# Optimization experiments

Hardware: AMD Instinct MI355X
Metric: run time of the kernel (lower is better)

Reference implementation:

```python
import jax, jax.numpy as jnp
import numpy as np

N = 100000
E = 1600000
IN_DIM, HID, H_IN, OUT_DIM, H_OUT = 128, 32, 2, 1, 1
NEG_SLOPE = 0.2


def gat_conv(x, W, a_src, a_dst, b, src, dst, concat):
    """PyG-style GATConv. x:[N,F_in], W:[F_in,H*C], a_*:[H,C], b:[H*C] or [C]."""
    H, C = a_src.shape
    h = (x @ W).reshape(N, H, C)
    asrc = jnp.einsum('nhc,hc->nh', h, a_src)   # [N,H]
    adst = jnp.einsum('nhc,hc->nh', h, a_dst)   # [N,H]
    e = jax.nn.leaky_relu(asrc[src] + adst[dst], NEG_SLOPE)  # [E',H]
    # segment softmax over incoming edges of each destination node
    m = jax.ops.segment_max(e, dst, num_segments=N)
    p = jnp.exp(e - m[dst])
    s = jax.ops.segment_sum(p, dst, num_segments=N)
    alpha = p / s[dst]                           # [E',H]
    out = jax.ops.segment_sum(alpha[:, :, None] * h[src], dst, num_segments=N)  # [N,H,C]
    out = out.reshape(N, H * C) if concat else out.mean(axis=1)
    return out + b


def setup_inputs() -> dict:
    key = jax.random.key(0)
    ks = jax.random.split(key, 16)
    def glorot(k, shape):
        fan = sum(shape[-2:]) if len(shape) > 1 else shape[-1]
        return jax.random.normal(k, shape, jnp.float32) * (2.0 / fan) ** 0.5
    node_attrs = jax.random.normal(ks[0], (N, IN_DIM), jnp.float32)
    edge_index = jax.random.randint(ks[1], (2, E), 0, N, jnp.int64 if jax.config.jax_enable_x64 else jnp.int32)
    params = {
        'W_in':  glorot(ks[2], (IN_DIM, H_IN * HID)),
        'a_src_in': glorot(ks[3], (H_IN, HID)),
        'a_dst_in': glorot(ks[4], (H_IN, HID)),
        'b_in':  jnp.zeros((H_IN * HID,), jnp.float32),
        'W_mid': glorot(ks[5], (H_IN * HID, H_IN * HID)),
        'a_src_mid': glorot(ks[6], (H_IN, HID)),
        'a_dst_mid': glorot(ks[7], (H_IN, HID)),
        'b_mid': jnp.zeros((H_IN * HID,), jnp.float32),
        'W_out': glorot(ks[8], (H_IN * HID, H_OUT * OUT_DIM)),
        'a_src_out': glorot(ks[9], (H_OUT, OUT_DIM)),
        'a_dst_out': glorot(ks[10], (H_OUT, OUT_DIM)),
        'b_out': jnp.zeros((OUT_DIM,), jnp.float32),
    }
    return {'node_attrs': node_attrs, 'edge_index': edge_index, **params}


def reference(node_attrs, edge_index,
              W_in, a_src_in, a_dst_in, b_in,
              W_mid, a_src_mid, a_dst_mid, b_mid,
              W_out, a_src_out, a_dst_out, b_out):
    # add self loops (PyG GATConv default add_self_loops=True)
    loops = jnp.arange(N, dtype=edge_index.dtype)
    src = jnp.concatenate([edge_index[0], loops])
    dst = jnp.concatenate([edge_index[1], loops])

    x = gat_conv(node_attrs, W_in, a_src_in, a_dst_in, b_in, src, dst, True)
    initial_x = x
    x = jax.nn.elu(x)
    for _ in range(6):  # conv_mid reused 6 times with SHARED weights, as in source
        x = gat_conv(x, W_mid, a_src_mid, a_dst_mid, b_mid, src, dst, True) + initial_x
        x = jax.nn.elu(x)
    x = gat_conv(x, W_out, a_src_out, a_dst_out, b_out, src, dst, False)
    return jax.nn.sigmoid(x)
```

## Files before the change

### kernel.cpp

```cpp
#include <hip/hip_runtime.h>
#include <hip/hip_fp16.h>
#include <cmath>

#define NN 100000
#define EE 1600000
#define TOTE (EE + NN)
#define SHIFT 10
#define NBUK 98
#define CAPB 18432
#define SLACK 5632
#define SPAN (TOTE + NBUK * SLACK)
#define PCAP2 40

typedef _Float16 half8_t __attribute__((ext_vector_type(8)));
typedef _Float16 half4_t __attribute__((ext_vector_type(4)));
typedef float float4_t __attribute__((ext_vector_type(4)));

__device__ __forceinline__ float lrelu(float v) { return v > 0.f ? v : 0.2f * v; }

__global__ __launch_bounds__(256) void binA(const int* __restrict__ src, const int* __restrict__ dst,
                                            int* __restrict__ gcur, int* __restrict__ region) {
    __shared__ int cnt[NBUK], gbase[NBUK], pos[NBUK];
    int t = threadIdx.x;
    if (t < NBUK) cnt[t] = 0;
    __syncthreads();
    const int CH = (TOTE + gridDim.x - 1) / gridDim.x;
    int lo = blockIdx.x * CH;
    int hi = lo + CH; if (hi > TOTE) hi = TOTE;
    for (int e = lo + t; e < hi; e += 256) {
        int d = (e < EE) ? dst[e] : (e - EE);
        atomicAdd(&cnt[d >> SHIFT], 1);
    }
    __syncthreads();
    if (t < NBUK) {
        gbase[t] = atomicAdd(&gcur[t], cnt[t]);
        pos[t] = 0;
    }
    __syncthreads();
    for (int e = lo + t; e < hi; e += 256) {
        int s, d;
        if (e < EE) { s = src[e]; d = dst[e]; }
        else        { s = e - EE; d = s; }
        int b = d >> SHIFT;
        int k = atomicAdd(&pos[b], 1);
        region[(size_t)b * CAPB + gbase[b] + k] = (s << SHIFT) | (d & 1023);
    }
}

__global__ __launch_bounds__(1024) void binB(const int* __restrict__ region, const int* __restrict__ gcur,
                                             int2* __restrict__ rng, int* __restrict__ esrc) {
    __shared__ int ncur[1024];
    __shared__ int wsum[16];
    __shared__ int sg[NBUK];
    __shared__ int sBase;
    int b = blockIdx.x, t = threadIdx.x;
    int n0 = b << SHIFT;
    if (t < NBUK) sg[t] = gcur[t];
    ncur[t] = 0;
    __syncthreads();
    if (t == 0) {
        int run = 0;
        for (int bb = 0; bb < b; ++bb) run += sg[bb] + SLACK;
        sBase = run;
    }
    int cntE = gcur[b];
    const int* reg = region + (size_t)b * CAPB;
    __syncthreads();
    for (int i = t; i < cntE; i += 1024)
        atomicAdd(&ncur[reg[i] & 1023], 1);
    int base = sBase;
    __syncthreads();
    int v = ncur[t];
    int vp = (v + 7) & ~7;
    __syncthreads();
    int incl = vp;
    for (int off = 1; off < 64; off <<= 1) {
        int u = __shfl_up(incl, off);
        if ((t & 63) >= off) incl += u;
    }
    if ((t & 63) == 63) wsum[t >> 6] = incl;
    __syncthreads();
    if (t < 16) {
        int w = wsum[t];
        int winc = w;
        for (int off = 1; off < 16; off <<= 1) {
            int u = __shfl_up(winc, off);
            if (t >= off) winc += u;
        }
        wsum[t] = winc - w;
    }
    __syncthreads();
    int excl = incl - vp + wsum[t >> 6];
    int start = base + excl;
    int n = n0 + t;
    if (n < NN) rng[n] = make_int2(start, v);
    ncur[t] = start;
    __syncthreads();
    for (int i = t; i < cntE; i += 1024) {
        int p = reg[i];
        int local = p & 1023;
        int k = atomicAdd(&ncur[local], 1);
        esrc[k] = p >> SHIFT;
    }
    __syncthreads();
    if (n < NN) {
        for (int k = start + v; k < start + vp; ++k) esrc[k] = 0;
    }
}

__global__ __launch_bounds__(256) void degHist(const int2* __restrict__ rng, int* __restrict__ hist) {
    __shared__ int cnt[64];
    int t = threadIdx.x;
    if (t < 64) cnt[t] = 0;
    __syncthreads();
    int n = blockIdx.x * 256 + t;
    if (n < NN) {
        int d = rng[n].y; if (d > 63) d = 63;
        atomicAdd(&cnt[d], 1);
    }
    __syncthreads();
    if (t < 64 && cnt[t]) atomicAdd(&hist[t], cnt[t]);
}

__global__ void degScan(const int* __restrict__ hist, int* __restrict__ off) {
    int t = threadIdx.x;
    int v = hist[t];
    int incl = v;
    for (int o = 1; o < 64; o <<= 1) {
        int u = __shfl_up(incl, o);
        if (t >= o) incl += u;
    }
    off[t] = incl - v;
}

__global__ __launch_bounds__(256) void degSort(const int2* __restrict__ rng, int* __restrict__ off,
                                               int* __restrict__ perm) {
    __shared__ int cnt[64], base[64], pos[64];
    int t = threadIdx.x;
    if (t < 64) cnt[t] = 0;
    __syncthreads();
    int n = blockIdx.x * 256 + t;
    int d = 63;
    if (n < NN) {
        d = rng[n].y; if (d > 63) d = 63;
        atomicAdd(&cnt[d], 1);
    }
    __syncthreads();
    if (t < 64) { base[t] = atomicAdd(&off[t], cnt[t]); pos[t] = 0; }
    __syncthreads();
    if (n < NN) {
        int k = atomicAdd(&pos[d], 1);
        perm[base[d] + k] = n;
    }
}

__global__ __launch_bounds__(256) void mkInvRng(const int* __restrict__ perm, const int2* __restrict__ rng,
                                                int* __restrict__ inv, int2* __restrict__ rng2) {
    int i = blockIdx.x * 256 + threadIdx.x;
    if (i < NN) {
        int p = perm[i];
        inv[p] = i;
        rng2[i] = rng[p];
    }
}

__global__ __launch_bounds__(256) void xlat(const int* __restrict__ esrc, const int* __restrict__ inv,
                                            int* __restrict__ esrc2) {
    int k = blockIdx.x * 256 + threadIdx.x;
    if (k < SPAN) {
        unsigned v = (unsigned)esrc[k];
        if (v >= NN) v = 0;
        esrc2[k] = inv[v];
    }
}

__global__ void prepW(const float* __restrict__ Wg, _Float16* __restrict__ Wp) {
    int t = threadIdx.x;
    for (int i = t; i < 64 * 72; i += 256) {
        int row = i / 72, col = i - row * 72;
        _Float16 v = (_Float16)0.f;
        if (col < 64) {
            int k = (col & 3) * 16 + (col >> 2);
            v = (_Float16)Wg[k * 64 + row];
        }
        Wp[i] = v;
    }
}

template <int K, bool F32IN>
__global__ __launch_bounds__(256) void gemm_attn(const void* __restrict__ Xv, const float* __restrict__ W,
                                                 const float* __restrict__ a_src, const float* __restrict__ a_dst,
                                                 _Float16* __restrict__ H, float* __restrict__ asrc,
                                                 float* __restrict__ adst) {
    __shared__ _Float16 wt[64][K + 8];
    int t = threadIdx.x;
    for (int it = 0; it < K / 16; ++it) {
        int idx4 = it * 256 + t;
        int k = idx4 >> 4;
        int n4 = (idx4 * 4) & 63;
        int ks = F32IN ? k : ((k & 15) * 4 + (k >> 4));
        float4 v = *(const float4*)(W + (size_t)idx4 * 4);
        wt[n4 + 0][ks] = (_Float16)v.x;
        wt[n4 + 1][ks] = (_Float16)v.y;
        wt[n4 + 2][ks] = (_Float16)v.z;
        wt[n4 + 3][ks] = (_Float16)v.w;
    }
    __syncthreads();

    int row0 = blockIdx.x * 64;
    int wr = (t >> 6) * 16;
    int lane = t & 63;
    int m = lane & 15;
    int q = lane >> 4;

    int rowA = row0 + wr + m;
    if (rowA >= NN) rowA = NN - 1;

    float4_t acc[4] = { {0,0,0,0}, {0,0,0,0}, {0,0,0,0}, {0,0,0,0} };
#pragma unroll
    for (int kc = 0; kc < K / 32; ++kc) {
        half8_t av;
        if (F32IN) {
            const float* xrow = (const float*)Xv + (size_t)rowA * K + q * 8;
            float4 u0 = *(const float4*)(xrow + kc * 32);
            float4 u1 = *(const float4*)(xrow + kc * 32 + 4);
            av[0] = (_Float16)u0.x; av[1] = (_Float16)u0.y;
            av[2] = (_Float16)u0.z; av[3] = (_Float16)u0.w;
            av[4] = (_Float16)u1.x; av[5] = (_Float16)u1.y;
            av[6] = (_Float16)u1.z; av[7] = (_Float16)u1.w;
        } else {
            const _Float16* xrow = (const _Float16*)Xv + (size_t)rowA * K + q * 8;
            av = *(const half8_t*)(xrow + kc * 32);
        }
#pragma unroll
        for (int c = 0; c < 4; ++c) {
            half8_t bv = *(const half8_t*)&wt[c * 16 + m][kc * 32 + q * 8];
            acc[c] = __builtin_amdgcn_mfma_f32_16x16x32_f16(av, bv, acc[c], 0, 0, 0);
        }
    }

#pragma unroll
    for (int r = 0; r < 4; ++r) {
        int row = row0 + wr + q * 4 + r;
        if (row < NN) {
            half4_t hv = { (_Float16)acc[0][r], (_Float16)acc[1][r],
                           (_Float16)acc[2][r], (_Float16)acc[3][r] };
            *(half4_t*)(H + (size_t)row * 64 + m * 4) = hv;
        }
    }

    float as0 = a_src[m], as1 = a_src[16 + m], as2 = a_src[32 + m], as3 = a_src[48 + m];
    float ad0 = a_dst[m], ad1 = a_dst[16 + m], ad2 = a_dst[32 + m], ad3 = a_dst[48 + m];
#pragma unroll
    for (int r = 0; r < 4; ++r) {
        float s0 = acc[0][r] * as0 + acc[1][r] * as1;
        float s1 = acc[2][r] * as2 + acc[3][r] * as3;
        float d0 = acc[0][r] * ad0 + acc[1][r] * ad1;
        float d1 = acc[2][r] * ad2 + acc[3][r] * ad3;
#pragma unroll
        for (int mk = 1; mk < 16; mk <<= 1) {
            s0 += __shfl_xor(s0, mk);
            s1 += __shfl_xor(s1, mk);
            d0 += __shfl_xor(d0, mk);
            d1 += __shfl_xor(d1, mk);
        }
        int row = row0 + wr + q * 4 + r;
        if (m == 0 && row < NN) {
            asrc[2 * row + 0] = s0;
            asrc[2 * row + 1] = s1;
            adst[2 * row + 0] = d0;
            adst[2 * row + 1] = d1;
        }
    }
}

struct Acc8 { float a[8]; float l0, l1; };

__device__ __forceinline__ void acc4(Acc8& A, float4 p0, float4 p1, float4 p2, float4 p3,
                                     half8_t h0, half8_t h1, half8_t h2, half8_t h3) {
    A.l0 += p0.x + p1.x + p2.x + p3.x;
    A.l1 += p0.y + p1.y + p2.y + p3.y;
#pragma unroll
    for (int q = 0; q < 8; ++q) {
        float w0 = (q & 2) ? p0.y : p0.x;
        float w1 = (q & 2) ? p1.y : p1.x;
        float w2 = (q & 2) ? p2.y : p2.x;
        float w3 = (q & 2) ? p3.y : p3.x;
        A.a[q] += w0 * (float)h0[q] + w1 * (float)h1[q]
                + w2 * (float)h2[q] + w3 * (float)h3[q];
    }
}

template <int MODE, bool SLOT>
__global__ __launch_bounds__(256, 6) void edge_agg(const int* __restrict__ perm, const int2* __restrict__ rngP,
                                                const int* __restrict__ esrcP, const _Float16* __restrict__ h,
                                                const float* __restrict__ asrc, const float* __restrict__ adst,
                                                const float* __restrict__ bias, _Float16* __restrict__ ixbuf,
                                                const _Float16* __restrict__ Wp, const float* __restrict__ asg,
                                                const float* __restrict__ adg, _Float16* __restrict__ hN,
                                                float* __restrict__ asrcN, float* __restrict__ adstN,
                                                const float* __restrict__ Wo, const float* __restrict__ a_s,
                                                const float* __restrict__ a_d, float2* __restrict__ ho2,
                                                float* __restrict__ adst_o) {
    __shared__ float4 pLDS[4][8][PCAP2 + 1];
    int bid = gridDim.x - 1 - blockIdx.x;
    int tid = threadIdx.x;
    int wq = tid >> 6;
    int lane = tid & 63;
    int g = lane >> 3;
    int c8 = lane & 7;

    int slot = (bid * 4 + wq) * 8 + g;
    int mn;
    if constexpr (SLOT) mn = slot; else mn = perm[slot];
    int2 r = rngP[mn];
    int start = r.x, deg = r.y;
    int vp = (deg + 3) & ~3;
    if (vp > PCAP2) vp = PCAP2;
    float2 ad = *(const float2*)(adst + 2 * (size_t)mn);

    for (int j = c8; j < vp; j += 8) {
        float p0 = 0.f, p1 = 0.f;
        int s = 0;
        if (j < deg) {
            s = esrcP[start + j];
            float2 as = *(const float2*)(asrc + 2 * (size_t)s);
            p0 = __expf(fminf(lrelu(as.x + ad.x), 60.f));
            p1 = __expf(fminf(lrelu(as.y + ad.y), 60.f));
        }
        pLDS[wq][g][j] = make_float4(p0, p1, __int_as_float(s), 0.f);
    }

    float bi[8];
#pragma unroll
    for (int q = 0; q < 8; ++q) bi[q] = bias[(q & 3) * 16 + 2 * c8 + (q >> 2)];
    half8_t iv = {};
    if constexpr (MODE != 0) iv = *(const half8_t*)(ixbuf + (size_t)slot * 64 + 8 * c8);
    float wo[8];
    float as0o = 0.f, ad0o = 0.f;
    if constexpr (MODE == 2) {
#pragma unroll
        for (int q = 0; q < 8; ++q) wo[q] = Wo[(q & 3) * 16 + 2 * c8 + (q >> 2)];
        as0o = a_s[0]; ad0o = a_d[0];
    }

    const float4* pb = &pLDS[wq][g][0];
    const _Float16* hb = h + 8 * c8;
    Acc8 A = {};
    float4 pc0 = pb[0], pc1 = pb[1], pc2 = pb[2], pc3 = pb[3];
    half8_t hc0 = *(const half8_t*)(hb + ((size_t)__float_as_int(pc0.z) << 6));
    half8_t hc1 = *(const half8_t*)(hb + ((size_t)__float_as_int(pc1.z) << 6));
    half8_t hc2 = *(const half8_t*)(hb + ((size_t)__float_as_int(pc2.z) << 6));
    half8_t hc3 = *(const half8_t*)(hb + ((size_t)__float_as_int(pc3.z) << 6));
    for (int j = 4; j < vp; j += 4) {
        float4 pn0 = pb[j], pn1 = pb[j + 1], pn2 = pb[j + 2], pn3 = pb[j + 3];
        acc4(A, pc0, pc1, pc2, pc3, hc0, hc1, hc2, hc3);
        half8_t hn0 = *(const half8_t*)(hb + ((size_t)__float_as_int(pn0.z) << 6));
        half8_t hn1 = *(const half8_t*)(hb + ((size_t)__float_as_int(pn1.z) << 6));
        half8_t hn2 = *(const half8_t*)(hb + ((size_t)__float_as_int(pn2.z) << 6));
        half8_t hn3 = *(const half8_t*)(hb + ((size_t)__float_as_int(pn3.z) << 6));
        pc0 = pn0; pc1 = pn1; pc2 = pn2; pc3 = pn3;
        hc0 = hn0; hc1 = hn1; hc2 = hn2; hc3 = hn3;
    }
    acc4(A, pc0, pc1, pc2, pc3, hc0, hc1, hc2, hc3);

    float inv0 = 1.f / A.l0, inv1 = 1.f / A.l1;
    float t[8];
#pragma unroll
    for (int q = 0; q < 8; ++q) t[q] = A.a[q] * ((q & 2) ? inv1 : inv0) + bi[q];
    if constexpr (MODE == 0) {
        half8_t o;
#pragma unroll
        for (int q = 0; q < 8; ++q) o[q] = (_Float16)t[q];
        *(half8_t*)(ixbuf + (size_t)slot * 64 + 8 * c8) = o;
    } else {
#pragma unroll
        for (int q = 0; q < 8; ++q) t[q] += (float)iv[q];
    }
#pragma unroll
    for (int q = 0; q < 8; ++q) t[q] = t[q] > 0.f ? t[q] : __expf(t[q]) - 1.f;

    if constexpr (MODE != 2) {
        _Float16* xs = (_Float16*)&pLDS[wq][0][0];
        half8_t xv;
#pragma unroll
        for (int q = 0; q < 8; ++q) xv[q] = (_Float16)t[q];
        *(half8_t*)(xs + g * 72 + 8 * c8) = xv;
        int m = lane & 15, qq = lane >> 4;
        half8_t bf0[4], bf1[4];
#pragma unroll
        for (int c = 0; c < 4; ++c) {
            const _Float16* wrow = Wp + (c * 16 + m) * 72 + qq * 8;
            bf0[c] = *(const half8_t*)(wrow);
            bf1[c] = *(const half8_t*)(wrow + 32);
        }
        const _Float16* xrow = xs + (m & 7) * 72 + qq * 8;
        half8_t a0 = *(const half8_t*)(xrow);
        half8_t a1 = *(const half8_t*)(xrow + 32);
        float4_t ag[4] = { {0,0,0,0}, {0,0,0,0}, {0,0,0,0}, {0,0,0,0} };
#pragma unroll
        for (int c = 0; c < 4; ++c) {
            ag[c] = __builtin_amdgcn_mfma_f32_16x16x32_f16(a0, bf0[c], ag[c], 0, 0, 0);
            ag[c] = __builtin_amdgcn_mfma_f32_16x16x32_f16(a1, bf1[c], ag[c], 0, 0, 0);
        }
        int base = (bid * 4 + wq) * 8;
#pragma unroll
        for (int rr = 0; rr < 4; ++rr) {
            if (qq < 2) {
                int nr = base + qq * 4 + rr;
                half4_t hv = { (_Float16)ag[0][rr], (_Float16)ag[1][rr],
                               (_Float16)ag[2][rr], (_Float16)ag[3][rr] };
                *(half4_t*)(hN + (size_t)nr * 64 + m * 4) = hv;
            }
        }
        float gs0 = asg[m], gs1 = asg[16 + m], gs2 = asg[32 + m], gs3 = asg[48 + m];
        float gd0 = adg[m], gd1 = adg[16 + m], gd2 = adg[32 + m], gd3 = adg[48 + m];
#pragma unroll
        for (int rr = 0; rr < 4; ++rr) {
            float s0 = ag[0][rr] * gs0 + ag[1][rr] * gs1;
            float s1 = ag[2][rr] * gs2 + ag[3][rr] * gs3;
            float d0 = ag[0][rr] * gd0 + ag[1][rr] * gd1;
            float d1 = ag[2][rr] * gd2 + ag[3][rr] * gd3;
#pragma unroll
            for (int mk = 1; mk < 16; mk <<= 1) {
                s0 += __shfl_xor(s0, mk);
                s1 += __shfl_xor(s1, mk);
                d0 += __shfl_xor(d0, mk);
                d1 += __shfl_xor(d1, mk);
            }
            if (m == 0 && qq < 2) {
                int nr = base + qq * 4 + rr;
                asrcN[2 * nr + 0] = s0;
                asrcN[2 * nr + 1] = s1;
                adstN[2 * nr + 0] = d0;
                adstN[2 * nr + 1] = d1;
            }
        }
    } else {
        float v = 0.f;
#pragma unroll
        for (int q = 0; q < 8; ++q) v += t[q] * wo[q];
        v += __shfl_xor(v, 1);
        v += __shfl_xor(v, 2);
        v += __shfl_xor(v, 4);
        if (c8 == 0) {
            ho2[slot] = make_float2(v, v * as0o);
            adst_o[slot] = v * ad0o;
        }
    }
}

__global__ __launch_bounds__(256) void edge_agg_out(const int* __restrict__ perm, const int2* __restrict__ rng2,
                                                    const int* __restrict__ esrc2, const float2* __restrict__ ho2,
                                                    const float* __restrict__ adst_o, const float* __restrict__ b_out,
                                                    float* __restrict__ out) {
    int bid = gridDim.x - 1 - blockIdx.x;
    int wq = threadIdx.x >> 6;
    int lane = threadIdx.x & 63;
    int g = lane >> 3;
    int c8 = lane & 7;
    int slot = (bid * 4 + wq) * 8 + g;
    int2 r = rng2[slot];
    float adv = adst_o[slot];
    float l = 0.f, acc = 0.f;
    for (int j = c8; j < r.y; j += 8) {
        int s = esrc2[r.x + j];
        float2 v = ho2[s];
        float p = __expf(fminf(lrelu(v.y + adv), 60.f));
        l += p;
        acc = fmaf(p, v.x, acc);
    }
    l += __shfl_xor(l, 1); acc += __shfl_xor(acc, 1);
    l += __shfl_xor(l, 2); acc += __shfl_xor(acc, 2);
    l += __shfl_xor(l, 4); acc += __shfl_xor(acc, 4);
    if (c8 == 0) out[perm[slot]] = 1.f / (1.f + __expf(-(acc / l + b_out[0])));
}

extern "C" void kernel_launch(void* const* d_in, const int* in_sizes, int n_in,
                              void* d_out, int out_size, void* d_ws, size_t ws_size,
                              hipStream_t stream) {
    const float* node_attrs = (const float*)d_in[0];
    const int*   edge_index = (const int*)d_in[1];
    const float* W_in      = (const float*)d_in[2];
    const float* a_src_in  = (const float*)d_in[3];
    const float* a_dst_in  = (const float*)d_in[4];
    const float* b_in      = (const float*)d_in[5];
    const float* W_mid     = (const float*)d_in[6];
    const float* a_src_mid = (const float*)d_in[7];
    const float* a_dst_mid = (const float*)d_in[8];
    const float* b_mid     = (const float*)d_in[9];
    const float* W_out     = (const float*)d_in[10];
    const float* a_src_out = (const float*)d_in[11];
    const float* a_dst_out = (const float*)d_in[12];
    const float* b_out     = (const float*)d_in[13];
    float* out = (float*)d_out;

    const int* srcArr = edge_index;
    const int* dstArr = edge_index + EE;

    char* w = (char*)d_ws;
    auto alloc = [&](size_t bytes) { void* p = (void*)w; w += (bytes + 255) & ~(size_t)255; return p; };
    int2*  rng        = (int2*)alloc((size_t)NN * 8);
    int2*  rng2       = (int2*)alloc((size_t)NN * 8);
    int*   gcur       = (int*)alloc((size_t)NBUK * 4);
    int*   region     = (int*)alloc((size_t)NBUK * CAPB * 4);
    int*   esrc       = (int*)alloc((size_t)SPAN * 4);
    int*   esrc2      = (int*)alloc((size_t)SPAN * 4);
    _Float16* hA      = (_Float16*)alloc((size_t)NN * 64 * 2);
    _Float16* hB      = (_Float16*)alloc((size_t)NN * 64 * 2);
    _Float16* ixbuf   = (_Float16*)alloc((size_t)NN * 64 * 2);
    float* asA        = (float*)alloc((size_t)NN * 2 * 4);
    float* adA        = (float*)alloc((size_t)NN * 2 * 4);
    float* asB        = (float*)alloc((size_t)NN * 2 * 4);
    float* adB        = (float*)alloc((size_t)NN * 2 * 4);
    float2* ho2       = (float2*)alloc((size_t)NN * 8);
    float* adst_o     = (float*)alloc((size_t)NN * 4);
    int*   perm       = (int*)alloc((size_t)NN * 4);
    int*   invp       = (int*)alloc((size_t)NN * 4);
    int*   hist       = (int*)alloc(64 * 4);
    int*   off        = (int*)alloc(64 * 4);
    _Float16* wperm   = (_Float16*)alloc((size_t)64 * 72 * 2);

    hipMemsetAsync(gcur, 0, NBUK * 4, stream);
    hipMemsetAsync(hist, 0, 64 * 4, stream);
    binA<<<256, 256, 0, stream>>>(srcArr, dstArr, gcur, region);
    binB<<<NBUK, 1024, 0, stream>>>(region, gcur, rng, esrc);

    int nBlk = (NN + 255) / 256;
    degHist<<<nBlk, 256, 0, stream>>>(rng, hist);
    degScan<<<1, 64, 0, stream>>>(hist, off);
    degSort<<<nBlk, 256, 0, stream>>>(rng, off, perm);
    mkInvRng<<<nBlk, 256, 0, stream>>>(perm, rng, invp, rng2);
    xlat<<<(SPAN + 255) / 256, 256, 0, stream>>>(esrc, invp, esrc2);

    prepW<<<1, 256, 0, stream>>>(W_mid, wperm);

    int gemmBlocks = (NN + 63) / 64;
    int aggBlocks = NN / 32;

    gemm_attn<128, true><<<gemmBlocks, 256, 0, stream>>>(node_attrs, W_in, a_src_in, a_dst_in, hA, asA, adA);

    edge_agg<0, false><<<aggBlocks, 256, 0, stream>>>(perm, rng, esrc, hA, asA, adA, b_in, ixbuf,
                                                      wperm, a_src_mid, a_dst_mid, hB, asB, adB,
                                                      nullptr, nullptr, nullptr, nullptr, nullptr);

    for (int l = 0; l < 5; ++l) {
        _Float16* hs = (l & 1) ? hA : hB;  float* ass = (l & 1) ? asA : asB;  float* ads = (l & 1) ? adA : adB;
        _Float16* hd = (l & 1) ? hB : hA;  float* asd = (l & 1) ? asB : asA;  float* add = (l & 1) ? adB : adA;
        edge_agg<1, true><<<aggBlocks, 256, 0, stream>>>(perm, rng2, esrc2, hs, ass, ads, b_mid, ixbuf,
                                                         wperm, a_src_mid, a_dst_mid, hd, asd, add,
                                                         nullptr, nullptr, nullptr, nullptr, nullptr);
    }
    edge_agg<2, true><<<aggBlocks, 256, 0, stream>>>(perm, rng2, esrc2, hA, asA, adA, b_mid, ixbuf,
                                                     nullptr, nullptr, nullptr, nullptr, nullptr, nullptr,
                                                     W_out, a_src_out, a_dst_out, ho2, adst_o);

    edge_agg_out<<<aggBlocks, 256, 0, stream>>>(perm, rng2, esrc2, ho2, adst_o, b_out, out);
}
```

Before: 512.6 us.

## Merge preprocessing kernels and run first layer entirely in permuted order

The degree histogram now accumulates inside binB, and the scan and weight prep share one launch. The inverse permutation and permuted ranges are written directly in degSort. The source-index translation runs as extra blocks of the first GEMM kernel, which now reads input rows through perm so the first edge_agg can use permuted indices as well. This removes several small kernel launches and intermediate passes. The cost is more coupling between stages, and a GEMM that gathers its input rows instead of reading them contiguously.

Result: faster. 496.1 us (-3.2%).

```diff
diff --git a/kernel.cpp b/kernel.cpp
--- a/kernel.cpp
+++ b/kernel.cpp
@@ -11,6 +11,8 @@
 #define SLACK 5632
 #define SPAN (TOTE + NBUK * SLACK)
 #define PCAP2 40
+#define GB 1563
+#define XB ((SPAN + 255) / 256)
 
 typedef _Float16 half8_t __attribute__((ext_vector_type(8)));
 typedef _Float16 half4_t __attribute__((ext_vector_type(4)));
@@ -48,14 +50,17 @@
 }
 
 __global__ __launch_bounds__(1024) void binB(const int* __restrict__ region, const int* __restrict__ gcur,
-                                             int2* __restrict__ rng, int* __restrict__ esrc) {
+                                             int2* __restrict__ rng, int* __restrict__ esrc,
+                                             int* __restrict__ hist) {
     __shared__ int ncur[1024];
     __shared__ int wsum[16];
     __shared__ int sg[NBUK];
+    __shared__ int dh[64];
     __shared__ int sBase;
     int b = blockIdx.x, t = threadIdx.x;
     int n0 = b << SHIFT;
     if (t < NBUK) sg[t] = gcur[t];
+    if (t < 64) dh[t] = 0;
     ncur[t] = 0;
     __syncthreads();
     if (t == 0) {
@@ -72,6 +77,7 @@
     __syncthreads();
     int v = ncur[t];
     int vp = (v + 7) & ~7;
+    if (n0 + t < NN) atomicAdd(&dh[v > 63 ? 63 : v], 1);
     __syncthreads();
     int incl = vp;
     for (int off = 1; off < 64; off <<= 1) {
@@ -106,43 +112,48 @@
     if (n < NN) {
         for (int k = start + v; k < start + vp; ++k) esrc[k] = 0;
     }
-}
-
-__global__ __launch_bounds__(256) void degHist(const int2* __restrict__ rng, int* __restrict__ hist) {
-    __shared__ int cnt[64];
+    if (t < 64) atomicAdd(&hist[t], dh[t]);
+}
+
+__global__ __launch_bounds__(256) void scanPrep(const int* __restrict__ hist, int* __restrict__ off,
+                                                const float* __restrict__ Wg, _Float16* __restrict__ Wp) {
     int t = threadIdx.x;
-    if (t < 64) cnt[t] = 0;
-    __syncthreads();
-    int n = blockIdx.x * 256 + t;
-    if (n < NN) {
-        int d = rng[n].y; if (d > 63) d = 63;
-        atomicAdd(&cnt[d], 1);
-    }
-    __syncthreads();
-    if (t < 64 && cnt[t]) atomicAdd(&hist[t], cnt[t]);
-}
-
-__global__ void degScan(const int* __restrict__ hist, int* __restrict__ off) {
-    int t = threadIdx.x;
-    int v = hist[t];
-    int incl = v;
-    for (int o = 1; o < 64; o <<= 1) {
-        int u = __shfl_up(incl, o);
-        if (t >= o) incl += u;
-    }
-    off[t] = incl - v;
+    if (blockIdx.x == 0) {
+        if (t < 64) {
+            int v = hist[t];
+            int incl = v;
+            for (int o = 1; o < 64; o <<= 1) {
+                int u = __shfl_up(incl, o);
+                if (t >= o) incl += u;
+            }
+            off[t] = incl - v;
+        }
+    } else {
+        for (int i = t; i < 64 * 72; i += 256) {
+            int row = i / 72, col = i - row * 72;
+            _Float16 v = (_Float16)0.f;
+            if (col < 64) {
+                int k = (col & 3) * 16 + (col >> 2);
+                v = (_Float16)Wg[k * 64 + row];
+            }
+            Wp[i] = v;
+        }
+    }
 }
 
 __global__ __launch_bounds__(256) void degSort(const int2* __restrict__ rng, int* __restrict__ off,
-                                               int* __restrict__ perm) {
+                                               int* __restrict__ perm, int* __restrict__ inv,
+                                               int2* __restrict__ rng2) {
     __shared__ int cnt[64], base[64], pos[64];
     int t = threadIdx.x;
     if (t < 64) cnt[t] = 0;
     __syncthreads();
     int n = blockIdx.x * 256 + t;
     int d = 63;
+    int2 r = make_int2(0, 0);
     if (n < NN) {
-        d = rng[n].y; if (d > 63) d = 63;
+        r = rng[n];
+        d = r.y > 63 ? 63 : r.y;
         atomicAdd(&cnt[d], 1);
     }
     __syncthreads();
@@ -150,64 +161,45 @@
     __syncthreads();
     if (n < NN) {
         int k = atomicAdd(&pos[d], 1);
-        perm[base[d] + k] = n;
-    }
-}
-
-__global__ __launch_bounds__(256) void mkInvRng(const int* __restrict__ perm, const int2* __restrict__ rng,
-                                                int* __restrict__ inv, int2* __restrict__ rng2) {
-    int i = blockIdx.x * 256 + threadIdx.x;
-    if (i < NN) {
-        int p = perm[i];
-        inv[p] = i;
-        rng2[i] = rng[p];
-    }
-}
-
-__global__ __launch_bounds__(256) void xlat(const int* __restrict__ esrc, const int* __restrict__ inv,
-                                            int* __restrict__ esrc2) {
-    int k = blockIdx.x * 256 + threadIdx.x;
-    if (k < SPAN) {
-        unsigned v = (unsigned)esrc[k];
-        if (v >= NN) v = 0;
-        esrc2[k] = inv[v];
-    }
-}
-
-__global__ void prepW(const float* __restrict__ Wg, _Float16* __restrict__ Wp) {
+        int slot = base[d] + k;
+        perm[slot] = n;
+        inv[n] = slot;
+        rng2[slot] = r;
+    }
+}
+
+__global__ __launch_bounds__(256) void gemm128_xlat(const float* __restrict__ X, const float* __restrict__ W,
+                                                    const int* __restrict__ perm,
+                                                    const float* __restrict__ a_src, const float* __restrict__ a_dst,
+                                                    _Float16* __restrict__ H, float* __restrict__ asrc,
+                                                    float* __restrict__ adst,
+                                                    const int* __restrict__ esrc, const int* __restrict__ inv,
+                                                    int* __restrict__ esrc2) {
+    __shared__ _Float16 wt[64][136];
+    int bid = blockIdx.x;
     int t = threadIdx.x;
-    for (int i = t; i < 64 * 72; i += 256) {
-        int row = i / 72, col = i - row * 72;
-        _Float16 v = (_Float16)0.f;
-        if (col < 64) {
-            int k = (col & 3) * 16 + (col >> 2);
-            v = (_Float16)Wg[k * 64 + row];
-        }
-        Wp[i] = v;
-    }
-}
-
-template <int K, bool F32IN>
-__global__ __launch_bounds__(256) void gemm_attn(const void* __restrict__ Xv, const float* __restrict__ W,
-                                                 const float* __restrict__ a_src, const float* __restrict__ a_dst,
-                                                 _Float16* __restrict__ H, float* __restrict__ asrc,
-                                                 float* __restrict__ adst) {
-    __shared__ _Float16 wt[64][K + 8];
-    int t = threadIdx.x;
-    for (int it = 0; it < K / 16; ++it) {
+    if (bid >= GB) {
+        int k = (bid - GB) * 256 + t;
+        if (k < SPAN) {
+            unsigned v = (unsigned)esrc[k];
+            if (v >= NN) v = 0;
+            esrc2[k] = inv[v];
+        }
+        return;
+    }
+    for (int it = 0; it < 8; ++it) {
         int idx4 = it * 256 + t;
         int k = idx4 >> 4;
         int n4 = (idx4 * 4) & 63;
-        int ks = F32IN ? k : ((k & 15) * 4 + (k >> 4));
         float4 v = *(const float4*)(W + (size_t)idx4 * 4);
-        wt[n4 + 0][ks] = (_Float16)v.x;
-        wt[n4 + 1][ks] = (_Float16)v.y;
-        wt[n4 + 2][ks] = (_Float16)v.z;
-        wt[n4 + 3][ks] = (_Float16)v.w;
-    }
-    __syncthreads();
-
-    int row0 = blockIdx.x * 64;
+        wt[n4 + 0][k] = (_Float16)v.x;
+        wt[n4 + 1][k] = (_Float16)v.y;
+        wt[n4 + 2][k] = (_Float16)v.z;
+        wt[n4 + 3][k] = (_Float16)v.w;
+    }
+    __syncthreads();
+
+    int row0 = bid * 64;
     int wr = (t >> 6) * 16;
     int lane = t & 63;
     int m = lane & 15;
@@ -215,23 +207,19 @@
 
     int rowA = row0 + wr + m;
     if (rowA >= NN) rowA = NN - 1;
+    int srow = perm[rowA];
 
     float4_t acc[4] = { {0,0,0,0}, {0,0,0,0}, {0,0,0,0}, {0,0,0,0} };
 #pragma unroll
-    for (int kc = 0; kc < K / 32; ++kc) {
+    for (int kc = 0; kc < 4; ++kc) {
+        const float* xrow = X + (size_t)srow * 128 + q * 8;
+        float4 u0 = *(const float4*)(xrow + kc * 32);
+        float4 u1 = *(const float4*)(xrow + kc * 32 + 4);
         half8_t av;
-        if (F32IN) {
-            const float* xrow = (const float*)Xv + (size_t)rowA * K + q * 8;
-            float4 u0 = *(const float4*)(xrow + kc * 32);
-            float4 u1 = *(const float4*)(xrow + kc * 32 + 4);
-            av[0] = (_Float16)u0.x; av[1] = (_Float16)u0.y;
-            av[2] = (_Float16)u0.z; av[3] = (_Float16)u0.w;
-            av[4] = (_Float16)u1.x; av[5] = (_Float16)u1.y;
-            av[6] = (_Float16)u1.z; av[7] = (_Float16)u1.w;
-        } else {
-            const _Float16* xrow = (const _Float16*)Xv + (size_t)rowA * K + q * 8;
-            av = *(const half8_t*)(xrow + kc * 32);
-        }
+        av[0] = (_Float16)u0.x; av[1] = (_Float16)u0.y;
+        av[2] = (_Float16)u0.z; av[3] = (_Float16)u0.w;
+        av[4] = (_Float16)u1.x; av[5] = (_Float16)u1.y;
+        av[6] = (_Float16)u1.z; av[7] = (_Float16)u1.w;
 #pragma unroll
         for (int c = 0; c < 4; ++c) {
             half8_t bv = *(const half8_t*)&wt[c * 16 + m][kc * 32 + q * 8];
@@ -291,9 +279,9 @@
     }
 }
 
-template <int MODE, bool SLOT>
-__global__ __launch_bounds__(256, 6) void edge_agg(const int* __restrict__ perm, const int2* __restrict__ rngP,
-                                                const int* __restrict__ esrcP, const _Float16* __restrict__ h,
+template <int MODE>
+__global__ __launch_bounds__(256, 6) void edge_agg(const int2* __restrict__ rng2,
+                                                const int* __restrict__ esrc2, const _Float16* __restrict__ h,
                                                 const float* __restrict__ asrc, const float* __restrict__ adst,
                                                 const float* __restrict__ bias, _Float16* __restrict__ ixbuf,
                                                 const _Float16* __restrict__ Wp, const float* __restrict__ asg,
@@ -311,19 +299,17 @@
     int c8 = lane & 7;
 
     int slot = (bid * 4 + wq) * 8 + g;
-    int mn;
-    if constexpr (SLOT) mn = slot; else mn = perm[slot];
-    int2 r = rngP[mn];
+    int2 r = rng2[slot];
     int start = r.x, deg = r.y;
     int vp = (deg + 3) & ~3;
     if (vp > PCAP2) vp = PCAP2;
-    float2 ad = *(const float2*)(adst + 2 * (size_t)mn);
+    float2 ad = *(const float2*)(adst + 2 * (size_t)slot);
 
     for (int j = c8; j < vp; j += 8) {
         float p0 = 0.f, p1 = 0.f;
         int s = 0;
         if (j < deg) {
-            s = esrcP[start + j];
+            s = esrc2[start + j];
             float2 as = *(const float2*)(asrc + 2 * (size_t)s);
             p0 = __expf(fminf(lrelu(as.x + ad.x), 60.f));
             p1 = __expf(fminf(lrelu(as.y + ad.y), 60.f));
@@ -524,36 +510,31 @@
     hipMemsetAsync(gcur, 0, NBUK * 4, stream);
     hipMemsetAsync(hist, 0, 64 * 4, stream);
     binA<<<256, 256, 0, stream>>>(srcArr, dstArr, gcur, region);
-    binB<<<NBUK, 1024, 0, stream>>>(region, gcur, rng, esrc);
-
+    binB<<<NBUK, 1024, 0, stream>>>(region, gcur, rng, esrc, hist);
+
+    scanPrep<<<2, 256, 0, stream>>>(hist, off, W_mid, wperm);
     int nBlk = (NN + 255) / 256;
-    degHist<<<nBlk, 256, 0, stream>>>(rng, hist);
-    degScan<<<1, 64, 0, stream>>>(hist, off);
-    degSort<<<nBlk, 256, 0, stream>>>(rng, off, perm);
-    mkInvRng<<<nBlk, 256, 0, stream>>>(perm, rng, invp, rng2);
-    xlat<<<(SPAN + 255) / 256, 256, 0, stream>>>(esrc, invp, esrc2);
-
-    prepW<<<1, 256, 0, stream>>>(W_mid, wperm);
-
-    int gemmBlocks = (NN + 63) / 64;
+    degSort<<<nBlk, 256, 0, stream>>>(rng, off, perm, invp, rng2);
+
     int aggBlocks = NN / 32;
 
-    gemm_attn<128, true><<<gemmBlocks, 256, 0, stream>>>(node_attrs, W_in, a_src_in, a_dst_in, hA, asA, adA);
-
-    edge_agg<0, false><<<aggBlocks, 256, 0, stream>>>(perm, rng, esrc, hA, asA, adA, b_in, ixbuf,
-                                                      wperm, a_src_mid, a_dst_mid, hB, asB, adB,
-                                                      nullptr, nullptr, nullptr, nullptr, nullptr);
+    gemm128_xlat<<<GB + XB, 256, 0, stream>>>(node_attrs, W_in, perm, a_src_in, a_dst_in,
+                                              hA, asA, adA, esrc, invp, esrc2);
+
+    edge_agg<0><<<aggBlocks, 256, 0, stream>>>(rng2, esrc2, hA, asA, adA, b_in, ixbuf,
+                                               wperm, a_src_mid, a_dst_mid, hB, asB, adB,
+                                               nullptr, nullptr, nullptr, nullptr, nullptr);
 
     for (int l = 0; l < 5; ++l) {
         _Float16* hs = (l & 1) ? hA : hB;  float* ass = (l & 1) ? asA : asB;  float* ads = (l & 1) ? adA : adB;
         _Float16* hd = (l & 1) ? hB : hA;  float* asd = (l & 1) ? asB : asA;  float* add = (l & 1) ? adB : adA;
-        edge_agg<1, true><<<aggBlocks, 256, 0, stream>>>(perm, rng2, esrc2, hs, ass, ads, b_mid, ixbuf,
-                                                         wperm, a_src_mid, a_dst_mid, hd, asd, add,
-                                                         nullptr, nullptr, nullptr, nullptr, nullptr);
-    }
-    edge_agg<2, true><<<aggBlocks, 256, 0, stream>>>(perm, rng2, esrc2, hA, asA, adA, b_mid, ixbuf,
-                                                     nullptr, nullptr, nullptr, nullptr, nullptr, nullptr,
-                                                     W_out, a_src_out, a_dst_out, ho2, adst_o);
+        edge_agg<1><<<aggBlocks, 256, 0, stream>>>(rng2, esrc2, hs, ass, ads, b_mid, ixbuf,
+                                                   wperm, a_src_mid, a_dst_mid, hd, asd, add,
+                                                   nullptr, nullptr, nullptr, nullptr, nullptr);
+    }
+    edge_agg<2><<<aggBlocks, 256, 0, stream>>>(rng2, esrc2, hA, asA, adA, b_mid, ixbuf,
+                                               nullptr, nullptr, nullptr, nullptr, nullptr, nullptr,
+                                               W_out, a_src_out, a_dst_out, ho2, adst_o);
 
     edge_agg_out<<<aggBlocks, 256, 0, stream>>>(perm, rng2, esrc2, ho2, adst_o, b_out, out);
 }
```
